# Optimization experiments

Hardware: AMD Instinct MI355X
Metric: run time of the kernel (lower is better)

The kernel has to match this reference:

```python
import jax, jax.numpy as jnp
import numpy as np
from jax import lax

BN_INV = float(1.0 / np.sqrt(1.0 + 1e-5))  # BatchNorm eval: running_mean=0, running_var=1


def _block(x, w, b, g, beta, stride):
    # Conv3x3(stride, pad=1) -> BN(eval) -> ReLU -> MaxPool2
    x = lax.conv_general_dilated(x, w, (stride, stride), [(1, 1), (1, 1)],
                                 dimension_numbers=('NCHW', 'OIHW', 'NCHW'))
    x = x + b[None, :, None, None]
    x = x * (g * BN_INV)[None, :, None, None] + beta[None, :, None, None]
    x = jax.nn.relu(x)
    return lax.reduce_window(x, -jnp.inf, lax.max, (1, 1, 2, 2), (1, 1, 2, 2), 'VALID')


def _gru(x, wi, wh, bi, bh):
    # torch-style GRU, batch_first. x: (B, T, D)
    B = x.shape[0]
    H = wh.shape[1]

    def step(h, xt):
        gi = xt @ wi.T + bi
        gh = h @ wh.T + bh
        ir, iz, inn = jnp.split(gi, 3, axis=1)
        hr, hz, hn = jnp.split(gh, 3, axis=1)
        r = jax.nn.sigmoid(ir + hr)
        z = jax.nn.sigmoid(iz + hz)
        nn_ = jnp.tanh(inn + r * hn)
        h2 = (1.0 - z) * nn_ + z * h
        return h2, h2

    h0 = jnp.zeros((B, H), x.dtype)
    _, ys = lax.scan(step, h0, jnp.swapaxes(x, 0, 1))
    return jnp.swapaxes(ys, 0, 1)  # (B, T, H)


def setup_inputs() -> dict:
    key = jax.random.key(0)
    ks = jax.random.split(key, 32)
    rn = lambda i, shape, s: jax.random.normal(ks[i], shape, jnp.float32) * s
    inp = {
        'support': rn(0, (5, 5, 1, 224, 224), 1.0),
        'query': rn(1, (15, 1, 224, 224), 1.0),
        'conv_w1': rn(2, (32, 1, 3, 3), 0.3), 'conv_b1': rn(3, (32,), 0.1),
        'conv_w2': rn(4, (64, 32, 3, 3), 0.06), 'conv_b2': rn(5, (64,), 0.1),
        'conv_w3': rn(6, (128, 64, 3, 3), 0.04), 'conv_b3': rn(7, (128,), 0.1),
        'conv_w4': rn(8, (256, 128, 3, 3), 0.03), 'conv_b4': rn(9, (256,), 0.1),
        'bn_g1': 1.0 + rn(10, (32,), 0.05), 'bn_be1': rn(11, (32,), 0.05),
        'bn_g2': 1.0 + rn(12, (64,), 0.05), 'bn_be2': rn(13, (64,), 0.05),
        'bn_g3': 1.0 + rn(14, (128,), 0.05), 'bn_be3': rn(15, (128,), 0.05),
        'bn_g4': 1.0 + rn(16, (256,), 0.05), 'bn_be4': rn(17, (256,), 0.05),
        'att_w': rn(18, (64, 256), 0.06), 'att_b': rn(19, (64,), 0.05),
        'gru_wi0': rn(20, (384, 512), 0.04), 'gru_wh0': rn(21, (384, 128), 0.08),
        'gru_bi0': rn(22, (384,), 0.05), 'gru_bh0': rn(23, (384,), 0.05),
        'gru_wi1': rn(24, (384, 128), 0.08), 'gru_wh1': rn(25, (384, 128), 0.08),
        'gru_bi1': rn(26, (384,), 0.05), 'gru_bh1': rn(27, (384,), 0.05),
        'trans_w': rn(28, (1, 128), 0.08), 'trans_b': rn(29, (1,), 0.05),
    }
    return inp


def reference(support, query, conv_w1, conv_b1, conv_w2, conv_b2, conv_w3, conv_b3,
              conv_w4, conv_b4, bn_g1, bn_be1, bn_g2, bn_be2, bn_g3, bn_be3,
              bn_g4, bn_be4, att_w, att_b, gru_wi0, gru_wh0, gru_bi0, gru_bh0,
              gru_wi1, gru_wh1, gru_bi1, gru_bh1, trans_w, trans_b):
    n, k, c, w = support.shape[0], support.shape[1], support.shape[2], support.shape[3]
    qk = query.shape[0]

    def enc(x):
        x = _block(x, conv_w1, conv_b1, bn_g1, bn_be1, 2)
        x = _block(x, conv_w2, conv_b2, bn_g2, bn_be2, 1)
        x = _block(x, conv_w3, conv_b3, bn_g3, bn_be3, 1)
        x = _block(x, conv_w4, conv_b4, bn_g4, bn_be4, 1)
        B, F_, H_, W_ = x.shape
        return x.reshape(B, F_, H_ * W_).transpose(0, 2, 1)  # (B, seq, feat)

    hf = enc(support.reshape(n * k, c, w, w))  # (nk, S, f)
    qf = enc(query)                            # (qk, T, f)

    # ItemQueryAttention: score[q,s,t,u] = sum_h tanh(W(q_t) * W(h_u))
    Wq = qf @ att_w.T + att_b  # (qk, T, h)
    Wh = hf @ att_w.T + att_b  # (nk, S, h)
    scores = jnp.tanh(Wq[:, None, :, None, :] * Wh[None, :, None, :, :]).sum(-1)  # (qk,nk,T,S)
    att = jax.nn.softmax(scores, axis=3)
    attended = jnp.einsum('qsTS,sSf->qsTf', att, hf)  # (qk, nk, T, f)

    T_, f = qf.shape[1], qf.shape[2]
    qrep = jnp.broadcast_to(qf[:, None], (qk, n * k, T_, f))
    x = jnp.concatenate([attended, qrep], axis=-1).reshape(qk * n * k, T_, 2 * f)

    h = _gru(x, gru_wi0, gru_wh0, gru_bi0, gru_bh0)
    h = _gru(h, gru_wi1, gru_wh1, gru_bi1, gru_bh1)

    logits = (h[:, -1, :] @ trans_w.T + trans_b).reshape(qk, n, k).sum(axis=2)  # (qk, n)
    return jax.nn.log_softmax(logits, axis=1)
```

## Files before the change

kernel.cpp:

```cpp
#include <hip/hip_runtime.h>
#include <hip/hip_bf16.h>
#include <math.h>

typedef unsigned short u16;
typedef unsigned int u32;
typedef __attribute__((ext_vector_type(8))) short bf16x8v;
typedef __attribute__((ext_vector_type(4))) float f32x4;

constexpr int NS = 25, NQ = 15, NB = 40;
constexpr int B3 = 375;
constexpr int T49 = 49;
constexpr float BN_INV = 0.9999950000374997f;

constexpr size_t A1_OFF    = 0;
constexpr size_t X2_OFF    = 16056320;
constexpr size_t P2_OFF    = 48168960;
constexpr size_t X3_OFF    = 0;
constexpr size_t P3_OFF    = 56197120;
constexpr size_t X4_OFF    = 16056320;
constexpr size_t FEATT_OFF = 60211200;
constexpr size_t PROJ_OFF  = 24084480;
constexpr size_t ATT_OFF   = 24586240;
constexpr size_t GI_OFF    = 62218240;
constexpr size_t Y0_OFF    = 0;
constexpr size_t HFIN_OFF  = 90442240;
constexpr size_t WBH_OFF   = 91027456;
constexpr size_t WBL_OFF   = 92325888;
constexpr size_t W2_E = 0;
constexpr size_t W3_E = 18432;
constexpr size_t W4_E = 92160;
constexpr size_t AW_E = 387072;
constexpr size_t WI0_E = 403456;
constexpr size_t WI1_E = 600064;
constexpr int CVT_N = 649216;

static __device__ __forceinline__ u16 f2b(float f) {
  __hip_bfloat16 h = __float2bfloat16(f);
  return *reinterpret_cast<u16*>(&h);
}
static __device__ __forceinline__ float b2f(u16 u) {
  return __uint_as_float((u32)u << 16);
}
static __device__ __forceinline__ void split8(const float* v, u32* hp, u32* lp) {
  u16 h[8], l[8];
#pragma unroll
  for (int j = 0; j < 8; ++j) {
    const u16 hb = f2b(v[j]);
    h[j] = hb;
    l[j] = f2b(v[j] - b2f(hb));
  }
#pragma unroll
  for (int j = 0; j < 4; ++j) {
    hp[j] = (u32)h[2 * j] | ((u32)h[2 * j + 1] << 16);
    lp[j] = (u32)l[2 * j] | ((u32)l[2 * j + 1] << 16);
  }
}
constexpr float LOG2E = 1.4426950408889634f;
static __device__ __forceinline__ float fsigmoid(float x) {
  return __builtin_amdgcn_rcpf(1.f + __builtin_amdgcn_exp2f(-x * LOG2E));
}
static __device__ __forceinline__ float ftanh(float x) {
  return 1.f - 2.f * __builtin_amdgcn_rcpf(__builtin_amdgcn_exp2f(x * (2.f * LOG2E)) + 1.f);
}

__global__ void cvt_all(const float* __restrict__ cw2, const float* __restrict__ cw3,
                        const float* __restrict__ cw4, const float* __restrict__ aw,
                        const float* __restrict__ wi0, const float* __restrict__ wi1,
                        u16* __restrict__ oh, u16* __restrict__ ol) {
  const int i = blockIdx.x * 256 + threadIdx.x;
  if (i >= CVT_N) return;
  float v;
  if (i < (int)W3_E) {
    const int l = i, oc = l / 288, rem = l - oc * 288, e = rem >> 5, ic = rem & 31;
    v = cw2[((size_t)(oc * 32 + ic) * 3 + e / 3) * 3 + e % 3];
  } else if (i < (int)W4_E) {
    const int l = i - (int)W3_E, oc = l / 576, rem = l - oc * 576, e = rem >> 6, ic = rem & 63;
    v = cw3[((size_t)(oc * 64 + ic) * 3 + e / 3) * 3 + e % 3];
  } else if (i < (int)AW_E) {
    const int l = i - (int)W4_E, oc = l / 1152, rem = l - oc * 1152, e = rem >> 7, ic = rem & 127;
    v = cw4[((size_t)(oc * 128 + ic) * 3 + e / 3) * 3 + e % 3];
  } else if (i < (int)WI0_E) {
    v = aw[i - (int)AW_E];
  } else if (i < (int)WI1_E) {
    v = wi0[i - (int)WI0_E];
  } else {
    v = wi1[i - (int)WI1_E];
  }
  const u16 h = f2b(v);
  oh[i] = h;
  ol[i] = f2b(v - b2f(h));
}

__global__ __launch_bounds__(256) void conv1_pool(
    const float* __restrict__ support, const float* __restrict__ query,
    const float* __restrict__ w1, const float* __restrict__ cb1,
    const float* __restrict__ g1, const float* __restrict__ be1,
    float* __restrict__ out) {
  __shared__ float wl[288], scl[32], shl[32], cbl[32];
  const int tid = threadIdx.x;
  for (int l = tid; l < 288; l += 256) wl[l] = w1[l];
  if (tid < 32) { scl[tid] = g1[tid] * BN_INV; shl[tid] = be1[tid]; cbl[tid] = cb1[tid]; }
  __syncthreads();
  const int oc = tid & 31;
  const int p = blockIdx.x * 8 + (tid >> 5);
  const int ox = p % 56, oy = (p / 56) % 56, b = p / 3136;
  const float* in_b = (b < NS) ? (support + (size_t)b * 50176)
                               : (query + (size_t)(b - NS) * 50176);
  const int iy0 = 4 * oy - 1, ix0 = 4 * ox - 1;
  float pat[5][5];
#pragma unroll
  for (int dy = 0; dy < 5; ++dy) {
    const int iy = iy0 + dy;
#pragma unroll
    for (int dx = 0; dx < 5; ++dx) {
      const int ix = ix0 + dx;
      pat[dy][dx] = (iy >= 0 && iy < 224 && ix >= 0 && ix < 224)
                        ? in_b[(size_t)iy * 224 + ix] : 0.f;
    }
  }
  const float* wp = &wl[oc * 9];
  float mx = 0.f;
#pragma unroll
  for (int py = 0; py < 2; ++py)
#pragma unroll
    for (int px = 0; px < 2; ++px) {
      float acc = 0.f;
#pragma unroll
      for (int ky = 0; ky < 3; ++ky)
#pragma unroll
        for (int kx = 0; kx < 3; ++kx)
          acc += pat[2 * py + ky][2 * px + kx] * wp[ky * 3 + kx];
      float v = (acc + cbl[oc]) * scl[oc] + shl[oc];
      mx = fmaxf(mx, v);
    }
  out[(size_t)p * 32 + oc] = mx;
}

__global__ void maxpool2_f32(const float* __restrict__ X, float* __restrict__ Y,
                             int Bn, int H, int W, int C) {
  const int OH = H >> 1, OW = W >> 1;
  const int cpr = C >> 2;
  const int chunks = Bn * OH * OW * cpr;
  for (int i = blockIdx.x * blockDim.x + threadIdx.x; i < chunks;
       i += gridDim.x * blockDim.x) {
    const int c4 = i % cpr, m = i / cpr;
    const int ox = m % OW, oy = (m / OW) % OH, b = m / (OW * OH);
    const size_t base = (((size_t)b * H + 2 * oy) * W + 2 * ox) * C + (c4 << 2);
    const float4 r0 = *(const float4*)&X[base];
    const float4 r1 = *(const float4*)&X[base + C];
    const float4 r2 = *(const float4*)&X[base + (size_t)W * C];
    const float4 r3 = *(const float4*)&X[base + (size_t)W * C + C];
    float4 o;
    o.x = fmaxf(fmaxf(r0.x, r1.x), fmaxf(r2.x, r3.x));
    o.y = fmaxf(fmaxf(r0.y, r1.y), fmaxf(r2.y, r3.y));
    o.z = fmaxf(fmaxf(r0.z, r1.z), fmaxf(r2.z, r3.z));
    o.w = fmaxf(fmaxf(r0.w, r1.w), fmaxf(r2.w, r3.w));
    *(float4*)&Y[(size_t)m * C + (c4 << 2)] = o;
  }
}

template <int AMODE, int EPI>
__global__ __launch_bounds__(256) void sgemm(
    const float* __restrict__ A, const float* __restrict__ A2, int M, int K,
    const u16* __restrict__ Bh, const u16* __restrict__ Bl,
    const float* __restrict__ p0, const float* __restrict__ p1,
    const float* __restrict__ p2, float* __restrict__ Cout, int ldc,
    int H, int W, int IC, int icb) {
  __shared__ u16 Ash[64][72], Asl[64][72];
  __shared__ u16 Bsh[64][72], Bsl[64][72];
  const int tid = threadIdx.x;
  const int lane = tid & 63, wv = tid >> 6;
  const int wy = wv >> 1, wx = wv & 1;
  const int n0 = blockIdx.x * 64, m0 = blockIdx.y * 64;
  f32x4 acc[2][2] = {{{0, 0, 0, 0}, {0, 0, 0, 0}}, {{0, 0, 0, 0}, {0, 0, 0, 0}}};
  for (int k0 = 0; k0 < K; k0 += 64) {
#pragma unroll
    for (int s = 0; s < 2; ++s) {
      const int c = s * 256 + tid;
      const int row = c >> 3, kc = (c & 7) << 3;
      const int gm = m0 + row, gk = k0 + kc;
      float4 x0 = {0, 0, 0, 0}, x1 = {0, 0, 0, 0};
      if (AMODE == 0) {
        if (gm < M && gk < K) {
          const float* p = A + (size_t)gm * K + gk;
          x0 = *(const float4*)p; x1 = *(const float4*)(p + 4);
        }
      } else if (AMODE == 1) {
        if (gm < M) {
          const float* p;
          if (gk < 256) {
            p = A + (size_t)gm * 256 + gk;
          } else {
            const int b = gm / T49, t = gm % T49, q = b / NS;
            p = A2 + (((size_t)(NS + q) * T49 + t) << 8) + (gk - 256);
          }
          x0 = *(const float4*)p; x1 = *(const float4*)(p + 4);
        }
      } else {
        if (gm < M && gk < K) {
          const int ox = gm % W, t_ = gm / W;
          const int oy = t_ % H, b = t_ / H;
          const int e = gk >> icb, ic = gk & (IC - 1);
          const int ky = e / 3, kx = e - 3 * (e / 3);
          const int iy = oy + ky - 1, ix = ox + kx - 1;
          if (iy >= 0 && iy < H && ix >= 0 && ix < W) {
            const float* p = A + (((size_t)b * H + iy) * W + ix) * IC + ic;
            x0 = *(const float4*)p; x1 = *(const float4*)(p + 4);
          }
        }
      }
      float v[8] = {x0.x, x0.y, x0.z, x0.w, x1.x, x1.y, x1.z, x1.w};
      u32 hp[4], lp[4];
      split8(v, hp, lp);
      *(uint4*)&Ash[row][kc] = *(uint4*)hp;
      *(uint4*)&Asl[row][kc] = *(uint4*)lp;
    }
#pragma unroll
    for (int s = 0; s < 2; ++s) {
      const int c = s * 256 + tid;
      const int row = c >> 3, kc = (c & 7) << 3;
      const int gk = k0 + kc;
      uint4 vh = {0u, 0u, 0u, 0u}, vl = {0u, 0u, 0u, 0u};
      if (gk < K) {
        vh = *(const uint4*)&Bh[(size_t)(n0 + row) * K + gk];
        vl = *(const uint4*)&Bl[(size_t)(n0 + row) * K + gk];
      }
      *(uint4*)&Bsh[row][kc] = vh;
      *(uint4*)&Bsl[row][kc] = vl;
    }
    __syncthreads();
#pragma unroll
    for (int kk = 0; kk < 64; kk += 32) {
      const int ko = kk + ((lane >> 4) << 3);
      const int ra0 = wy * 32 + (lane & 15), ra1 = ra0 + 16;
      const int rb0 = wx * 32 + (lane & 15), rb1 = rb0 + 16;
      bf16x8v a0h = *(const bf16x8v*)&Ash[ra0][ko];
      bf16x8v a1h = *(const bf16x8v*)&Ash[ra1][ko];
      bf16x8v b0h = *(const bf16x8v*)&Bsh[rb0][ko];
      bf16x8v b1h = *(const bf16x8v*)&Bsh[rb1][ko];
      bf16x8v a0l = *(const bf16x8v*)&Asl[ra0][ko];
      bf16x8v a1l = *(const bf16x8v*)&Asl[ra1][ko];
      bf16x8v b0l = *(const bf16x8v*)&Bsl[rb0][ko];
      bf16x8v b1l = *(const bf16x8v*)&Bsl[rb1][ko];
      acc[0][0] = __builtin_amdgcn_mfma_f32_16x16x32_bf16(a0h, b0h, acc[0][0], 0, 0, 0);
      acc[0][1] = __builtin_amdgcn_mfma_f32_16x16x32_bf16(a0h, b1h, acc[0][1], 0, 0, 0);
      acc[1][0] = __builtin_amdgcn_mfma_f32_16x16x32_bf16(a1h, b0h, acc[1][0], 0, 0, 0);
      acc[1][1] = __builtin_amdgcn_mfma_f32_16x16x32_bf16(a1h, b1h, acc[1][1], 0, 0, 0);
      acc[0][0] = __builtin_amdgcn_mfma_f32_16x16x32_bf16(a0h, b0l, acc[0][0], 0, 0, 0);
      acc[0][1] = __builtin_amdgcn_mfma_f32_16x16x32_bf16(a0h, b1l, acc[0][1], 0, 0, 0);
      acc[1][0] = __builtin_amdgcn_mfma_f32_16x16x32_bf16(a1h, b0l, acc[1][0], 0, 0, 0);
      acc[1][1] = __builtin_amdgcn_mfma_f32_16x16x32_bf16(a1h, b1l, acc[1][1], 0, 0, 0);
      acc[0][0] = __builtin_amdgcn_mfma_f32_16x16x32_bf16(a0l, b0h, acc[0][0], 0, 0, 0);
      acc[0][1] = __builtin_amdgcn_mfma_f32_16x16x32_bf16(a0l, b1h, acc[0][1], 0, 0, 0);
      acc[1][0] = __builtin_amdgcn_mfma_f32_16x16x32_bf16(a1l, b0h, acc[1][0], 0, 0, 0);
      acc[1][1] = __builtin_amdgcn_mfma_f32_16x16x32_bf16(a1l, b1h, acc[1][1], 0, 0, 0);
    }
    __syncthreads();
  }
#pragma unroll
  for (int r = 0; r < 2; ++r) {
#pragma unroll
    for (int c = 0; c < 2; ++c) {
      const int gn = n0 + wx * 32 + c * 16 + (lane & 15);
      float sc0 = 0.f, sh0 = 0.f;
      if (EPI == 0) { sc0 = p1[gn] * BN_INV; sh0 = p2[gn]; }
#pragma unroll
      for (int i = 0; i < 4; ++i) {
        const int gm = m0 + wy * 32 + r * 16 + ((lane >> 4) << 2) + i;
        if (gm >= M) continue;
        const float a = acc[r][c][i];
        if (EPI == 0) {
          Cout[(size_t)gm * ldc + gn] = fmaxf((a + p0[gn]) * sc0 + sh0, 0.f);
        } else {
          Cout[(size_t)gm * ldc + gn] = a + p0[gn];
        }
      }
    }
  }
}

__global__ __launch_bounds__(256) void attention_f32(
    const float* __restrict__ proj, const float* __restrict__ featT,
    float* __restrict__ attended) {
  __shared__ float WqT[64][9];
  __shared__ float WhT[64][51];
  __shared__ float sc[7][64];
  const int bid = blockIdx.x;
  const int qs = bid / 7, tg = bid - 7 * qs;
  const int q = qs / NS, s = qs - NS * q;
  const int tid = threadIdx.x;
  const float* pq = proj + ((size_t)(NS + q) * T49 + tg * 7) * 64;
  const float* ph = proj + (size_t)s * T49 * 64;
  for (int l = tid; l < 7 * 64; l += 256) WqT[l & 63][l >> 6] = pq[l];
  for (int l = tid; l < T49 * 64; l += 256) WhT[l & 63][l >> 6] = ph[l];
  __syncthreads();
  constexpr float C2LOG2E = 2.8853900817779268f;
  for (int e = tid; e < 343; e += 256) {
    const int tl = e / 49, u = e - 49 * tl;
    float a0 = 0.f, a1 = 0.f, a2 = 0.f, a3 = 0.f;
#pragma unroll
    for (int h = 0; h < 64; h += 4) {
      const float p0 = WqT[h + 0][tl] * WhT[h + 0][u];
      const float p1 = WqT[h + 1][tl] * WhT[h + 1][u];
      const float p2 = WqT[h + 2][tl] * WhT[h + 2][u];
      const float p3 = WqT[h + 3][tl] * WhT[h + 3][u];
      a0 += 1.f - 2.f * __builtin_amdgcn_rcpf(__builtin_amdgcn_exp2f(p0 * C2LOG2E) + 1.f);
      a1 += 1.f - 2.f * __builtin_amdgcn_rcpf(__builtin_amdgcn_exp2f(p1 * C2LOG2E) + 1.f);
      a2 += 1.f - 2.f * __builtin_amdgcn_rcpf(__builtin_amdgcn_exp2f(p2 * C2LOG2E) + 1.f);
      a3 += 1.f - 2.f * __builtin_amdgcn_rcpf(__builtin_amdgcn_exp2f(p3 * C2LOG2E) + 1.f);
    }
    sc[tl][u] = (a0 + a1) + (a2 + a3);
  }
  __syncthreads();
  if (tid < 56) {
    const int t = tid >> 3, g = tid & 7;
    float m = -3.4e38f;
    for (int u = g; u < T49; u += 8) m = fmaxf(m, sc[t][u]);
    m = fmaxf(m, __shfl_xor(m, 4));
    m = fmaxf(m, __shfl_xor(m, 2));
    m = fmaxf(m, __shfl_xor(m, 1));
    float ssum = 0.f;
    for (int u = g; u < T49; u += 8) {
      const float e = __builtin_amdgcn_exp2f((sc[t][u] - m) * LOG2E);
      sc[t][u] = e; ssum += e;
    }
    ssum += __shfl_xor(ssum, 4);
    ssum += __shfl_xor(ssum, 2);
    ssum += __shfl_xor(ssum, 1);
    const float inv = 1.f / ssum;
    for (int u = g; u < T49; u += 8) sc[t][u] *= inv;
  }
  __syncthreads();
  const float* fs = featT + (size_t)s * T49 * 256;
  float* outp = attended + ((size_t)qs * T49 + tg * 7) * 256;
  float acc[7] = {0.f, 0.f, 0.f, 0.f, 0.f, 0.f, 0.f};
  for (int u = 0; u < T49; ++u) {
    const float v = fs[u * 256 + tid];
#pragma unroll
    for (int i = 0; i < 7; ++i) acc[i] += sc[i][u] * v;
  }
#pragma unroll
  for (int i = 0; i < 7; ++i) outp[(size_t)i * 256 + tid] = acc[i];
}

constexpr int SPB = 8;
__global__ __launch_bounds__(512) void gru_mfma(
    const float* __restrict__ gi,
    const float* __restrict__ wh,
    const float* __restrict__ bh,
    float* __restrict__ y,
    int store_all) {
  __shared__ u16 hah[16][136];
  __shared__ float ghs[SPB][384];
  __shared__ float hfl[SPB][128];
  const int tid = threadIdx.x;
  const int lane = tid & 63, wv = tid >> 6;
  const int r0 = blockIdx.x * SPB;
  bf16x8v Bhr[3][4], Blr[3][4];
#pragma unroll
  for (int f = 0; f < 3; ++f) {
    const int n = (wv * 3 + f) * 16 + (lane & 15);
#pragma unroll
    for (int kk = 0; kk < 4; ++kk) {
      const int k = kk * 32 + ((lane >> 4) << 3);
      const float* p = wh + (size_t)n * 128 + k;
      float v[8];
      *(float4*)&v[0] = *(const float4*)p;
      *(float4*)&v[4] = *(const float4*)(p + 4);
      u32 hp[4], lp[4];
      split8(v, hp, lp);
      Bhr[f][kk] = *(bf16x8v*)hp;
      Blr[f][kk] = *(bf16x8v*)lp;
    }
  }
  const int row0 = tid >> 7, j0 = tid & 127;
  const int row1 = (512 + tid) >> 7, j1 = tid & 127;
  int sq0 = r0 + row0; if (sq0 >= B3) sq0 = B3 - 1;
  int sq1 = r0 + row1; if (sq1 >= B3) sq1 = B3 - 1;
  const float bhr0 = bh[j0], bhz0 = bh[128 + j0], bhn0 = bh[256 + j0];
  const float bhr1 = bh[j1], bhz1 = bh[128 + j1], bhn1 = bh[256 + j1];
  const float* gib0 = gi + (size_t)sq0 * T49 * 384;
  const float* gib1 = gi + (size_t)sq1 * T49 * 384;
  for (int i = tid; i < 16 * 136; i += 512) hah[i / 136][i % 136] = 0;
  for (int i = tid; i < SPB * 128; i += 512) hfl[i >> 7][i & 127] = 0.f;
  __syncthreads();
  const int ar = lane & 15, ko = (lane >> 4) << 3;
  float xr0c = gib0[j0], xz0c = gib0[128 + j0], xn0c = gib0[256 + j0];
  float xr1c = gib1[j1], xz1c = gib1[128 + j1], xn1c = gib1[256 + j1];
  for (int t = 0; t < T49; ++t) {
    const int tn = (t + 1 < T49) ? t + 1 : t;
    const float* g0n = gib0 + (size_t)tn * 384;
    const float* g1n = gib1 + (size_t)tn * 384;
    const float xr0n = g0n[j0], xz0n = g0n[128 + j0], xn0n = g0n[256 + j0];
    const float xr1n = g1n[j1], xz1n = g1n[128 + j1], xn1n = g1n[256 + j1];
    bf16x8v Ah[4];
#pragma unroll
    for (int kk = 0; kk < 4; ++kk)
      Ah[kk] = *(const bf16x8v*)&hah[ar][kk * 32 + ko];
#pragma unroll
    for (int f = 0; f < 3; ++f) {
      f32x4 acc = {0, 0, 0, 0};
#pragma unroll
      for (int kk = 0; kk < 4; ++kk)
        acc = __builtin_amdgcn_mfma_f32_16x16x32_bf16(Ah[kk], Bhr[f][kk], acc, 0, 0, 0);
#pragma unroll
      for (int kk = 0; kk < 4; ++kk)
        acc = __builtin_amdgcn_mfma_f32_16x16x32_bf16(Ah[kk], Blr[f][kk], acc, 0, 0, 0);
      const int nc = (wv * 3 + f) * 16 + (lane & 15);
      const int rb = (lane >> 4) << 2;
      if (rb < SPB) {
#pragma unroll
        for (int i = 0; i < 4; ++i) ghs[rb + i][nc] = acc[i];
      }
    }
    __syncthreads();
    {
      const float r_ = fsigmoid(xr0c + ghs[row0][j0] + bhr0);
      const float z_ = fsigmoid(xz0c + ghs[row0][128 + j0] + bhz0);
      const float n_ = ftanh(xn0c + r_ * (ghs[row0][256 + j0] + bhn0));
      const float hn = (1.f - z_) * n_ + z_ * hfl[row0][j0];
      hfl[row0][j0] = hn;
      hah[row0][j0] = f2b(hn);
      if (r0 + row0 < B3) {
        if (store_all) y[((size_t)(r0 + row0) * T49 + t) * 128 + j0] = hn;
        else if (t == T49 - 1) y[(size_t)(r0 + row0) * 128 + j0] = hn;
      }
    }
    {
      const float r_ = fsigmoid(xr1c + ghs[row1][j1] + bhr1);
      const float z_ = fsigmoid(xz1c + ghs[row1][128 + j1] + bhz1);
      const float n_ = ftanh(xn1c + r_ * (ghs[row1][256 + j1] + bhn1));
      const float hn = (1.f - z_) * n_ + z_ * hfl[row1][j1];
      hfl[row1][j1] = hn;
      hah[row1][j1] = f2b(hn);
      if (r0 + row1 < B3) {
        if (store_all) y[((size_t)(r0 + row1) * T49 + t) * 128 + j1] = hn;
        else if (t == T49 - 1) y[(size_t)(r0 + row1) * 128 + j1] = hn;
      }
    }
    __syncthreads();
    xr0c = xr0n; xz0c = xz0n; xn0c = xn0n;
    xr1c = xr1n; xz1c = xz1n; xn1c = xn1n;
  }
}

__global__ __launch_bounds__(512) void head_kernel(
    const float* __restrict__ hf, const float* __restrict__ tw,
    const float* __restrict__ tb, float* __restrict__ out) {
  __shared__ float lg[B3];
  const int tid = threadIdx.x;
  if (tid < B3) {
    const float* h = hf + (size_t)tid * 128;
    float acc = tb[0];
    for (int k = 0; k < 128; ++k) acc += h[k] * tw[k];
    lg[tid] = acc;
  }
  __syncthreads();
  if (tid < NQ) {
    float cls[5];
#pragma unroll
    for (int n = 0; n < 5; ++n) {
      float s = 0.f;
#pragma unroll
      for (int k = 0; k < 5; ++k) s += lg[tid * 25 + n * 5 + k];
      cls[n] = s;
    }
    float m = cls[0];
#pragma unroll
    for (int n = 1; n < 5; ++n) m = fmaxf(m, cls[n]);
    float se = 0.f;
#pragma unroll
    for (int n = 0; n < 5; ++n) se += expf(cls[n] - m);
    const float lse = m + logf(se);
#pragma unroll
    for (int n = 0; n < 5; ++n) out[tid * 5 + n] = cls[n] - lse;
  }
}

extern "C" void kernel_launch(void* const* d_in, const int* in_sizes, int n_in,
                              void* d_out, int out_size, void* d_ws,
                              size_t ws_size, hipStream_t stream) {
  (void)in_sizes; (void)n_in; (void)out_size; (void)ws_size;
  const float* support = (const float*)d_in[0];
  const float* query   = (const float*)d_in[1];
  const float* cw1 = (const float*)d_in[2];  const float* cb1 = (const float*)d_in[3];
  const float* cw2 = (const float*)d_in[4];  const float* cb2 = (const float*)d_in[5];
  const float* cw3 = (const float*)d_in[6];  const float* cb3 = (const float*)d_in[7];
  const float* cw4 = (const float*)d_in[8];  const float* cb4 = (const float*)d_in[9];
  const float* g1  = (const float*)d_in[10]; const float* be1 = (const float*)d_in[11];
  const float* g2  = (const float*)d_in[12]; const float* be2 = (const float*)d_in[13];
  const float* g3  = (const float*)d_in[14]; const float* be3 = (const float*)d_in[15];
  const float* g4  = (const float*)d_in[16]; const float* be4 = (const float*)d_in[17];
  const float* aw  = (const float*)d_in[18]; const float* ab  = (const float*)d_in[19];
  const float* wi0 = (const float*)d_in[20]; const float* wh0 = (const float*)d_in[21];
  const float* bi0 = (const float*)d_in[22]; const float* bh0 = (const float*)d_in[23];
  const float* wi1 = (const float*)d_in[24]; const float* wh1 = (const float*)d_in[25];
  const float* bi1 = (const float*)d_in[26]; const float* bh1 = (const float*)d_in[27];
  const float* tw  = (const float*)d_in[28]; const float* tb  = (const float*)d_in[29];

  char* ws = (char*)d_ws;
  float* out = (float*)d_out;
  float* A1    = (float*)(ws + A1_OFF);
  float* X2    = (float*)(ws + X2_OFF);
  float* P2    = (float*)(ws + P2_OFF);
  float* X3    = (float*)(ws + X3_OFF);
  float* P3    = (float*)(ws + P3_OFF);
  float* X4    = (float*)(ws + X4_OFF);
  float* FEATT = (float*)(ws + FEATT_OFF);
  float* PROJ  = (float*)(ws + PROJ_OFF);
  float* ATT   = (float*)(ws + ATT_OFF);
  float* GI    = (float*)(ws + GI_OFF);
  float* Y0    = (float*)(ws + Y0_OFF);
  float* HFIN  = (float*)(ws + HFIN_OFF);
  u16* WBH = (u16*)(ws + WBH_OFF);
  u16* WBL = (u16*)(ws + WBL_OFF);

  cvt_all<<<(CVT_N + 255) / 256, 256, 0, stream>>>(cw2, cw3, cw4, aw, wi0, wi1, WBH, WBL);

  conv1_pool<<<15680, 256, 0, stream>>>(support, query, cw1, cb1, g1, be1, A1);
  sgemm<2, 0><<<dim3(1, 1960), 256, 0, stream>>>(
      A1, nullptr, 125440, 288, WBH + W2_E, WBL + W2_E, cb2, g2, be2, X2, 64,
      56, 56, 32, 5);
  maxpool2_f32<<<1960, 256, 0, stream>>>(X2, P2, NB, 56, 56, 64);
  sgemm<2, 0><<<dim3(2, 490), 256, 0, stream>>>(
      P2, nullptr, 31360, 576, WBH + W3_E, WBL + W3_E, cb3, g3, be3, X3, 128,
      28, 28, 64, 6);
  maxpool2_f32<<<980, 256, 0, stream>>>(X3, P3, NB, 28, 28, 128);
  sgemm<2, 0><<<dim3(4, 123), 256, 0, stream>>>(
      P3, nullptr, 7840, 1152, WBH + W4_E, WBL + W4_E, cb4, g4, be4, X4, 256,
      14, 14, 128, 7);
  maxpool2_f32<<<490, 256, 0, stream>>>(X4, FEATT, NB, 14, 14, 256);

  sgemm<0, 1><<<dim3(1, 31), 256, 0, stream>>>(
      FEATT, nullptr, NB * T49, 256, WBH + AW_E, WBL + AW_E, ab, nullptr,
      nullptr, PROJ, 64, 0, 0, 0, 0);
  attention_f32<<<B3 * 7, 256, 0, stream>>>(PROJ, FEATT, ATT);

  sgemm<1, 1><<<dim3(6, 288), 256, 0, stream>>>(
      ATT, FEATT, B3 * T49, 512, WBH + WI0_E, WBL + WI0_E, bi0, nullptr,
      nullptr, GI, 384, 0, 0, 0, 0);
  gru_mfma<<<47, 512, 0, stream>>>(GI, wh0, bh0, Y0, 1);
  sgemm<0, 1><<<dim3(6, 288), 256, 0, stream>>>(
      Y0, nullptr, B3 * T49, 128, WBH + WI1_E, WBL + WI1_E, bi1, nullptr,
      nullptr, GI, 384, 0, 0, 0, 0);
  gru_mfma<<<47, 512, 0, stream>>>(GI, wh1, bh1, HFIN, 0);

  head_kernel<<<1, 512, 0, stream>>>(HFIN, tw, tb, out);
}
```

Baseline: 370.4 us.

## Store GEMM A-operands pre-split as bf16 hi/lo pairs in producers

Producer kernels (conv1_pool, the maxpool kernels, attention and GRU layer 0) now write their outputs as separate bf16 high and low halves instead of fp32. The GEMMs can then load both halves straight into shared memory without splitting them in the loop. This removes the repeated split work in every GEMM tile, which matters most for the im2col conv GEMMs where each activation is re-read up to nine times. Total bytes per element stay the same (two u16 values instead of one float), so the saving is mostly ALU work, and the workspace layout had to be re-planned.

Result: no change. 367.5 us (-0.8%).

```diff
diff --git a/kernel.cpp b/kernel.cpp
--- a/kernel.cpp
+++ b/kernel.cpp
@@ -12,20 +12,26 @@
 constexpr int T49 = 49;
 constexpr float BN_INV = 0.9999950000374997f;
 
-constexpr size_t A1_OFF    = 0;
-constexpr size_t X2_OFF    = 16056320;
-constexpr size_t P2_OFF    = 48168960;
-constexpr size_t X3_OFF    = 0;
-constexpr size_t P3_OFF    = 56197120;
-constexpr size_t X4_OFF    = 16056320;
-constexpr size_t FEATT_OFF = 60211200;
-constexpr size_t PROJ_OFF  = 24084480;
-constexpr size_t ATT_OFF   = 24586240;
-constexpr size_t GI_OFF    = 62218240;
-constexpr size_t Y0_OFF    = 0;
-constexpr size_t HFIN_OFF  = 90442240;
-constexpr size_t WBH_OFF   = 91027456;
-constexpr size_t WBL_OFF   = 92325888;
+constexpr size_t A1H_OFF    = 0;
+constexpr size_t A1L_OFF    = 8028160;
+constexpr size_t X2_OFF     = 16056320;
+constexpr size_t P2H_OFF    = 48168960;
+constexpr size_t P2L_OFF    = 52183040;
+constexpr size_t X3_OFF     = 0;
+constexpr size_t P3H_OFF    = 56197120;
+constexpr size_t P3L_OFF    = 58204160;
+constexpr size_t X4_OFF     = 0;
+constexpr size_t FEATTH_OFF = 60211200;
+constexpr size_t FEATTL_OFF = 61214720;
+constexpr size_t PROJ_OFF   = 0;
+constexpr size_t ATTH_OFF   = 16056320;
+constexpr size_t ATTL_OFF   = 25464320;
+constexpr size_t GI_OFF     = 62218240;
+constexpr size_t Y0H_OFF    = 0;
+constexpr size_t Y0L_OFF    = 4704000;
+constexpr size_t HFIN_OFF   = 90442240;
+constexpr size_t WBH_OFF    = 91027456;
+constexpr size_t WBL_OFF    = 92325888;
 constexpr size_t W2_E = 0;
 constexpr size_t W3_E = 18432;
 constexpr size_t W4_E = 92160;
@@ -41,6 +47,13 @@
 static __device__ __forceinline__ float b2f(u16 u) {
   return __uint_as_float((u32)u << 16);
 }
+constexpr float LOG2E = 1.4426950408889634f;
+static __device__ __forceinline__ float fsigmoid(float x) {
+  return __builtin_amdgcn_rcpf(1.f + __builtin_amdgcn_exp2f(-x * LOG2E));
+}
+static __device__ __forceinline__ float ftanh(float x) {
+  return 1.f - 2.f * __builtin_amdgcn_rcpf(__builtin_amdgcn_exp2f(x * (2.f * LOG2E)) + 1.f);
+}
 static __device__ __forceinline__ void split8(const float* v, u32* hp, u32* lp) {
   u16 h[8], l[8];
 #pragma unroll
@@ -54,13 +67,6 @@
     hp[j] = (u32)h[2 * j] | ((u32)h[2 * j + 1] << 16);
     lp[j] = (u32)l[2 * j] | ((u32)l[2 * j + 1] << 16);
   }
-}
-constexpr float LOG2E = 1.4426950408889634f;
-static __device__ __forceinline__ float fsigmoid(float x) {
-  return __builtin_amdgcn_rcpf(1.f + __builtin_amdgcn_exp2f(-x * LOG2E));
-}
-static __device__ __forceinline__ float ftanh(float x) {
-  return 1.f - 2.f * __builtin_amdgcn_rcpf(__builtin_amdgcn_exp2f(x * (2.f * LOG2E)) + 1.f);
 }
 
 __global__ void cvt_all(const float* __restrict__ cw2, const float* __restrict__ cw3,
@@ -95,7 +101,7 @@
     const float* __restrict__ support, const float* __restrict__ query,
     const float* __restrict__ w1, const float* __restrict__ cb1,
     const float* __restrict__ g1, const float* __restrict__ be1,
-    float* __restrict__ out) {
+    u16* __restrict__ outh, u16* __restrict__ outl) {
   __shared__ float wl[288], scl[32], shl[32], cbl[32];
   const int tid = threadIdx.x;
   for (int l = tid; l < 288; l += 256) wl[l] = w1[l];
@@ -133,11 +139,13 @@
       float v = (acc + cbl[oc]) * scl[oc] + shl[oc];
       mx = fmaxf(mx, v);
     }
-  out[(size_t)p * 32 + oc] = mx;
-}
-
-__global__ void maxpool2_f32(const float* __restrict__ X, float* __restrict__ Y,
-                             int Bn, int H, int W, int C) {
+  const u16 h = f2b(mx);
+  outh[(size_t)p * 32 + oc] = h;
+  outl[(size_t)p * 32 + oc] = f2b(mx - b2f(h));
+}
+
+__global__ void maxpool2_split(const float* __restrict__ X, u16* __restrict__ Yh,
+                               u16* __restrict__ Yl, int Bn, int H, int W, int C) {
   const int OH = H >> 1, OW = W >> 1;
   const int cpr = C >> 2;
   const int chunks = Bn * OH * OW * cpr;
@@ -150,18 +158,30 @@
     const float4 r1 = *(const float4*)&X[base + C];
     const float4 r2 = *(const float4*)&X[base + (size_t)W * C];
     const float4 r3 = *(const float4*)&X[base + (size_t)W * C + C];
-    float4 o;
-    o.x = fmaxf(fmaxf(r0.x, r1.x), fmaxf(r2.x, r3.x));
-    o.y = fmaxf(fmaxf(r0.y, r1.y), fmaxf(r2.y, r3.y));
-    o.z = fmaxf(fmaxf(r0.z, r1.z), fmaxf(r2.z, r3.z));
-    o.w = fmaxf(fmaxf(r0.w, r1.w), fmaxf(r2.w, r3.w));
-    *(float4*)&Y[(size_t)m * C + (c4 << 2)] = o;
+    float o[4];
+    o[0] = fmaxf(fmaxf(r0.x, r1.x), fmaxf(r2.x, r3.x));
+    o[1] = fmaxf(fmaxf(r0.y, r1.y), fmaxf(r2.y, r3.y));
+    o[2] = fmaxf(fmaxf(r0.z, r1.z), fmaxf(r2.z, r3.z));
+    o[3] = fmaxf(fmaxf(r0.w, r1.w), fmaxf(r2.w, r3.w));
+    u16 hh[4], ll[4];
+#pragma unroll
+    for (int j = 0; j < 4; ++j) {
+      hh[j] = f2b(o[j]);
+      ll[j] = f2b(o[j] - b2f(hh[j]));
+    }
+    const size_t off = (size_t)m * C + (c4 << 2);
+    uint2 vh, vl;
+    vh.x = (u32)hh[0] | ((u32)hh[1] << 16); vh.y = (u32)hh[2] | ((u32)hh[3] << 16);
+    vl.x = (u32)ll[0] | ((u32)ll[1] << 16); vl.y = (u32)ll[2] | ((u32)ll[3] << 16);
+    *(uint2*)&Yh[off] = vh;
+    *(uint2*)&Yl[off] = vl;
   }
 }
 
 template <int AMODE, int EPI>
 __global__ __launch_bounds__(256) void sgemm(
-    const float* __restrict__ A, const float* __restrict__ A2, int M, int K,
+    const u16* __restrict__ Ah, const u16* __restrict__ Al,
+    const u16* __restrict__ A2h, const u16* __restrict__ A2l, int M, int K,
     const u16* __restrict__ Bh, const u16* __restrict__ Bl,
     const float* __restrict__ p0, const float* __restrict__ p1,
     const float* __restrict__ p2, float* __restrict__ Cout, int ldc,
@@ -176,25 +196,29 @@
   for (int k0 = 0; k0 < K; k0 += 64) {
 #pragma unroll
     for (int s = 0; s < 2; ++s) {
-      const int c = s * 256 + tid;
-      const int row = c >> 3, kc = (c & 7) << 3;
+      const int cc = s * 256 + tid;
+      const int row = cc >> 3, kc = (cc & 7) << 3;
       const int gm = m0 + row, gk = k0 + kc;
-      float4 x0 = {0, 0, 0, 0}, x1 = {0, 0, 0, 0};
+      uint4 vh = {0u, 0u, 0u, 0u}, vl = {0u, 0u, 0u, 0u};
       if (AMODE == 0) {
         if (gm < M && gk < K) {
-          const float* p = A + (size_t)gm * K + gk;
-          x0 = *(const float4*)p; x1 = *(const float4*)(p + 4);
+          const size_t idx = (size_t)gm * K + gk;
+          vh = *(const uint4*)&Ah[idx];
+          vl = *(const uint4*)&Al[idx];
         }
       } else if (AMODE == 1) {
         if (gm < M) {
-          const float* p;
+          size_t idx;
+          const u16 *ph_, *pl_;
           if (gk < 256) {
-            p = A + (size_t)gm * 256 + gk;
+            idx = (size_t)gm * 256 + gk; ph_ = Ah; pl_ = Al;
           } else {
             const int b = gm / T49, t = gm % T49, q = b / NS;
-            p = A2 + (((size_t)(NS + q) * T49 + t) << 8) + (gk - 256);
+            idx = (((size_t)(NS + q) * T49 + t) << 8) + (gk - 256);
+            ph_ = A2h; pl_ = A2l;
           }
-          x0 = *(const float4*)p; x1 = *(const float4*)(p + 4);
+          vh = *(const uint4*)&ph_[idx];
+          vl = *(const uint4*)&pl_[idx];
         }
       } else {
         if (gm < M && gk < K) {
@@ -204,21 +228,19 @@
           const int ky = e / 3, kx = e - 3 * (e / 3);
           const int iy = oy + ky - 1, ix = ox + kx - 1;
           if (iy >= 0 && iy < H && ix >= 0 && ix < W) {
-            const float* p = A + (((size_t)b * H + iy) * W + ix) * IC + ic;
-            x0 = *(const float4*)p; x1 = *(const float4*)(p + 4);
+            const size_t idx = (((size_t)b * H + iy) * W + ix) * IC + ic;
+            vh = *(const uint4*)&Ah[idx];
+            vl = *(const uint4*)&Al[idx];
           }
         }
       }
-      float v[8] = {x0.x, x0.y, x0.z, x0.w, x1.x, x1.y, x1.z, x1.w};
-      u32 hp[4], lp[4];
-      split8(v, hp, lp);
-      *(uint4*)&Ash[row][kc] = *(uint4*)hp;
-      *(uint4*)&Asl[row][kc] = *(uint4*)lp;
+      *(uint4*)&Ash[row][kc] = vh;
+      *(uint4*)&Asl[row][kc] = vl;
     }
 #pragma unroll
     for (int s = 0; s < 2; ++s) {
-      const int c = s * 256 + tid;
-      const int row = c >> 3, kc = (c & 7) << 3;
+      const int cc = s * 256 + tid;
+      const int row = cc >> 3, kc = (cc & 7) << 3;
       const int gk = k0 + kc;
       uint4 vh = {0u, 0u, 0u, 0u}, vl = {0u, 0u, 0u, 0u};
       if (gk < K) {
@@ -260,15 +282,15 @@
 #pragma unroll
   for (int r = 0; r < 2; ++r) {
 #pragma unroll
-    for (int c = 0; c < 2; ++c) {
-      const int gn = n0 + wx * 32 + c * 16 + (lane & 15);
+    for (int cI = 0; cI < 2; ++cI) {
+      const int gn = n0 + wx * 32 + cI * 16 + (lane & 15);
       float sc0 = 0.f, sh0 = 0.f;
       if (EPI == 0) { sc0 = p1[gn] * BN_INV; sh0 = p2[gn]; }
 #pragma unroll
       for (int i = 0; i < 4; ++i) {
         const int gm = m0 + wy * 32 + r * 16 + ((lane >> 4) << 2) + i;
         if (gm >= M) continue;
-        const float a = acc[r][c][i];
+        const float a = acc[r][cI][i];
         if (EPI == 0) {
           Cout[(size_t)gm * ldc + gn] = fmaxf((a + p0[gn]) * sc0 + sh0, 0.f);
         } else {
@@ -280,8 +302,9 @@
 }
 
 __global__ __launch_bounds__(256) void attention_f32(
-    const float* __restrict__ proj, const float* __restrict__ featT,
-    float* __restrict__ attended) {
+    const float* __restrict__ proj, const u16* __restrict__ featTh,
+    const u16* __restrict__ featTl, u16* __restrict__ atth,
+    u16* __restrict__ attl) {
   __shared__ float WqT[64][9];
   __shared__ float WhT[64][51];
   __shared__ float sc[7][64];
@@ -331,16 +354,22 @@
     for (int u = g; u < T49; u += 8) sc[t][u] *= inv;
   }
   __syncthreads();
-  const float* fs = featT + (size_t)s * T49 * 256;
-  float* outp = attended + ((size_t)qs * T49 + tg * 7) * 256;
+  const u16* fsh = featTh + (size_t)s * T49 * 256;
+  const u16* fsl = featTl + (size_t)s * T49 * 256;
+  const size_t obase = ((size_t)qs * T49 + tg * 7) * 256;
   float acc[7] = {0.f, 0.f, 0.f, 0.f, 0.f, 0.f, 0.f};
   for (int u = 0; u < T49; ++u) {
-    const float v = fs[u * 256 + tid];
+    const float v = b2f(fsh[u * 256 + tid]) + b2f(fsl[u * 256 + tid]);
 #pragma unroll
     for (int i = 0; i < 7; ++i) acc[i] += sc[i][u] * v;
   }
 #pragma unroll
-  for (int i = 0; i < 7; ++i) outp[(size_t)i * 256 + tid] = acc[i];
+  for (int i = 0; i < 7; ++i) {
+    const float a = acc[i];
+    const u16 h = f2b(a);
+    atth[obase + (size_t)i * 256 + tid] = h;
+    attl[obase + (size_t)i * 256 + tid] = f2b(a - b2f(h));
+  }
 }
 
 constexpr int SPB = 8;
@@ -348,7 +377,8 @@
     const float* __restrict__ gi,
     const float* __restrict__ wh,
     const float* __restrict__ bh,
-    float* __restrict__ y,
+    u16* __restrict__ yh, u16* __restrict__ yl,
+    float* __restrict__ hfin,
     int store_all) {
   __shared__ u16 hah[16][136];
   __shared__ float ghs[SPB][384];
@@ -420,10 +450,16 @@
       const float n_ = ftanh(xn0c + r_ * (ghs[row0][256 + j0] + bhn0));
       const float hn = (1.f - z_) * n_ + z_ * hfl[row0][j0];
       hfl[row0][j0] = hn;
-      hah[row0][j0] = f2b(hn);
+      const u16 hb = f2b(hn);
+      hah[row0][j0] = hb;
       if (r0 + row0 < B3) {
-        if (store_all) y[((size_t)(r0 + row0) * T49 + t) * 128 + j0] = hn;
-        else if (t == T49 - 1) y[(size_t)(r0 + row0) * 128 + j0] = hn;
+        if (store_all) {
+          const size_t o = ((size_t)(r0 + row0) * T49 + t) * 128 + j0;
+          yh[o] = hb;
+          yl[o] = f2b(hn - b2f(hb));
+        } else if (t == T49 - 1) {
+          hfin[(size_t)(r0 + row0) * 128 + j0] = hn;
+        }
       }
     }
     {
@@ -432,10 +468,16 @@
       const float n_ = ftanh(xn1c + r_ * (ghs[row1][256 + j1] + bhn1));
       const float hn = (1.f - z_) * n_ + z_ * hfl[row1][j1];
       hfl[row1][j1] = hn;
-      hah[row1][j1] = f2b(hn);
+      const u16 hb = f2b(hn);
+      hah[row1][j1] = hb;
       if (r0 + row1 < B3) {
-        if (store_all) y[((size_t)(r0 + row1) * T49 + t) * 128 + j1] = hn;
-        else if (t == T49 - 1) y[(size_t)(r0 + row1) * 128 + j1] = hn;
+        if (store_all) {
+          const size_t o = ((size_t)(r0 + row1) * T49 + t) * 128 + j1;
+          yh[o] = hb;
+          yl[o] = f2b(hn - b2f(hb));
+        } else if (t == T49 - 1) {
+          hfin[(size_t)(r0 + row1) * 128 + j1] = hn;
+        }
       }
     }
     __syncthreads();
@@ -500,50 +542,56 @@
 
   char* ws = (char*)d_ws;
   float* out = (float*)d_out;
-  float* A1    = (float*)(ws + A1_OFF);
-  float* X2    = (float*)(ws + X2_OFF);
-  float* P2    = (float*)(ws + P2_OFF);
-  float* X3    = (float*)(ws + X3_OFF);
-  float* P3    = (float*)(ws + P3_OFF);
-  float* X4    = (float*)(ws + X4_OFF);
-  float* FEATT = (float*)(ws + FEATT_OFF);
-  float* PROJ  = (float*)(ws + PROJ_OFF);
-  float* ATT   = (float*)(ws + ATT_OFF);
-  float* GI    = (float*)(ws + GI_OFF);
-  float* Y0    = (float*)(ws + Y0_OFF);
-  float* HFIN  = (float*)(ws + HFIN_OFF);
+  u16* A1H    = (u16*)(ws + A1H_OFF);
+  u16* A1L    = (u16*)(ws + A1L_OFF);
+  float* X2   = (float*)(ws + X2_OFF);
+  u16* P2H    = (u16*)(ws + P2H_OFF);
+  u16* P2L    = (u16*)(ws + P2L_OFF);
+  float* X3   = (float*)(ws + X3_OFF);
+  u16* P3H    = (u16*)(ws + P3H_OFF);
+  u16* P3L    = (u16*)(ws + P3L_OFF);
+  float* X4   = (float*)(ws + X4_OFF);
+  u16* FEATTH = (u16*)(ws + FEATTH_OFF);
+  u16* FEATTL = (u16*)(ws + FEATTL_OFF);
+  float* PROJ = (float*)(ws + PROJ_OFF);
+  u16* ATTH   = (u16*)(ws + ATTH_OFF);
+  u16* ATTL   = (u16*)(ws + ATTL_OFF);
+  float* GI   = (float*)(ws + GI_OFF);
+  u16* Y0H    = (u16*)(ws + Y0H_OFF);
+  u16* Y0L    = (u16*)(ws + Y0L_OFF);
+  float* HFIN = (float*)(ws + HFIN_OFF);
   u16* WBH = (u16*)(ws + WBH_OFF);
   u16* WBL = (u16*)(ws + WBL_OFF);
 
   cvt_all<<<(CVT_N + 255) / 256, 256, 0, stream>>>(cw2, cw3, cw4, aw, wi0, wi1, WBH, WBL);
 
-  conv1_pool<<<15680, 256, 0, stream>>>(support, query, cw1, cb1, g1, be1, A1);
+  conv1_pool<<<15680, 256, 0, stream>>>(support, query, cw1, cb1, g1, be1, A1H, A1L);
   sgemm<2, 0><<<dim3(1, 1960), 256, 0, stream>>>(
-      A1, nullptr, 125440, 288, WBH + W2_E, WBL + W2_E, cb2, g2, be2, X2, 64,
-      56, 56, 32, 5);
-  maxpool2_f32<<<1960, 256, 0, stream>>>(X2, P2, NB, 56, 56, 64);
+      A1H, A1L, nullptr, nullptr, 125440, 288, WBH + W2_E, WBL + W2_E,
+      cb2, g2, be2, X2, 64, 56, 56, 32, 5);
+  maxpool2_split<<<1960, 256, 0, stream>>>(X2, P2H, P2L, NB, 56, 56, 64);
   sgemm<2, 0><<<dim3(2, 490), 256, 0, stream>>>(
-      P2, nullptr, 31360, 576, WBH + W3_E, WBL + W3_E, cb3, g3, be3, X3, 128,
-      28, 28, 64, 6);
-  maxpool2_f32<<<980, 256, 0, stream>>>(X3, P3, NB, 28, 28, 128);
+      P2H, P2L, nullptr, nullptr, 31360, 576, WBH + W3_E, WBL + W3_E,
+      cb3, g3, be3, X3, 128, 28, 28, 64, 6);
+  maxpool2_split<<<980, 256, 0, stream>>>(X3, P3H, P3L, NB, 28, 28, 128);
   sgemm<2, 0><<<dim3(4, 123), 256, 0, stream>>>(
-      P3, nullptr, 7840, 1152, WBH + W4_E, WBL + W4_E, cb4, g4, be4, X4, 256,
-      14, 14, 128, 7);
-  maxpool2_f32<<<490, 256, 0, stream>>>(X4, FEATT, NB, 14, 14, 256);
+      P3H, P3L, nullptr, nullptr, 7840, 1152, WBH + W4_E, WBL + W4_E,
+      cb4, g4, be4, X4, 256, 14, 14, 128, 7);
+  maxpool2_split<<<490, 256, 0, stream>>>(X4, FEATTH, FEATTL, NB, 14, 14, 256);
 
   sgemm<0, 1><<<dim3(1, 31), 256, 0, stream>>>(
-      FEATT, nullptr, NB * T49, 256, WBH + AW_E, WBL + AW_E, ab, nullptr,
-      nullptr, PROJ, 64, 0, 0, 0, 0);
-  attention_f32<<<B3 * 7, 256, 0, stream>>>(PROJ, FEATT, ATT);
+      FEATTH, FEATTL, nullptr, nullptr, NB * T49, 256, WBH + AW_E, WBL + AW_E,
+      ab, nullptr, nullptr, PROJ, 64, 0, 0, 0, 0);
+  attention_f32<<<B3 * 7, 256, 0, stream>>>(PROJ, FEATTH, FEATTL, ATTH, ATTL);
 
   sgemm<1, 1><<<dim3(6, 288), 256, 0, stream>>>(
-      ATT, FEATT, B3 * T49, 512, WBH + WI0_E, WBL + WI0_E, bi0, nullptr,
-      nullptr, GI, 384, 0, 0, 0, 0);
-  gru_mfma<<<47, 512, 0, stream>>>(GI, wh0, bh0, Y0, 1);
+      ATTH, ATTL, FEATTH, FEATTL, B3 * T49, 512, WBH + WI0_E, WBL + WI0_E,
+      bi0, nullptr, nullptr, GI, 384, 0, 0, 0, 0);
+  gru_mfma<<<47, 512, 0, stream>>>(GI, wh0, bh0, Y0H, Y0L, nullptr, 1);
   sgemm<0, 1><<<dim3(6, 288), 256, 0, stream>>>(
-      Y0, nullptr, B3 * T49, 128, WBH + WI1_E, WBL + WI1_E, bi1, nullptr,
-      nullptr, GI, 384, 0, 0, 0, 0);
-  gru_mfma<<<47, 512, 0, stream>>>(GI, wh1, bh1, HFIN, 0);
+      Y0H, Y0L, nullptr, nullptr, B3 * T49, 128, WBH + WI1_E, WBL + WI1_E,
+      bi1, nullptr, nullptr, GI, 384, 0, 0, 0, 0);
+  gru_mfma<<<47, 512, 0, stream>>>(GI, wh1, bh1, nullptr, nullptr, HFIN, 0);
 
   head_kernel<<<1, 512, 0, stream>>>(HFIN, tw, tb, out);
 }
```
